# Kernel tuning notes

Measured on AMD Instinct MI355X. Metric: run time of the kernel, lower is better.

Reference implementation:

```python
import jax, jax.numpy as jnp
import numpy as np
from jax import lax

N = 19
ACT_DIM = 12
_SRC = np.array([0,1,2,3,4,5,6,7,8,9,10,11,12,13,14,15,16,17,18,1,2,3,4,5,6,7,8,9,10,11,12,13,14,15,16,17], dtype=np.int64)
_DST = np.array([1,2,3,4,5,6,7,8,9,10,11,12,13,14,15,16,17,18,17,0,1,2,3,4,5,6,7,8,9,10,11,12,13,14,15,16], dtype=np.int64)
SRC = jnp.asarray(_SRC)
DST = jnp.asarray(_DST)
# GAT/GCN in PyG add self-loops by default
SRC_SL = jnp.concatenate([SRC, jnp.arange(N)])
DST_SL = jnp.concatenate([DST, jnp.arange(N)])


def _lin(v, W, b=None):
    y = v @ W.T
    return y + b if b is not None else y


def _minmax(v):
    return (v - v.min()) / (v.max() - v.min())


def _conv(x, w, b, pad):
    y = lax.conv_general_dilated(x, w, (2, 2), [(pad, pad), (pad, pad)], dimension_numbers=('NCHW', 'OIHW', 'NCHW'))
    return y + b[None, :, None, None]


def _sage_layer(h, lw, lb, rw):
    # SAGEConv(aggr='add'): lin_l(sum_{j->i} x_j) + lin_r(x_i); lin_r has no bias
    agg = jax.ops.segment_sum(h[SRC], DST, num_segments=N)
    return agg @ lw.T + lb + h @ rw.T


def _gat(h, W, a_s, a_d, b):
    # GATConv heads=1, leaky_relu slope 0.2, softmax over incoming edges (incl. self-loop)
    hh = h @ W.T
    es, ed = hh @ a_s, hh @ a_d
    e = jax.nn.leaky_relu(es[SRC_SL] + ed[DST_SL], 0.2)
    m = jax.ops.segment_max(e, DST_SL, num_segments=N)
    ex = jnp.exp(e - m[DST_SL])
    den = jax.ops.segment_sum(ex, DST_SL, num_segments=N)
    alpha = ex / den[DST_SL]
    return jax.ops.segment_sum(alpha[:, None] * hh[SRC_SL], DST_SL, num_segments=N) + b


def _gcn(h, W, b):
    # GCNConv(improved=True): A_hat = A + 2I, D^{-1/2} A_hat D^{-1/2}
    hh = h @ W.T
    w_e = jnp.concatenate([jnp.ones(SRC.shape[0], jnp.float32), 2.0 * jnp.ones(N, jnp.float32)])
    deg = jax.ops.segment_sum(w_e, DST_SL, num_segments=N)
    dinv = lax.rsqrt(deg)
    norm = dinv[SRC_SL] * dinv[DST_SL] * w_e
    return jax.ops.segment_sum(norm[:, None] * hh[SRC_SL], DST_SL, num_segments=N) + b


def setup_inputs() -> dict:
    ks = iter(jax.random.split(jax.random.key(0), 64))
    def nrm(*shape):
        return jax.random.normal(next(ks), shape, jnp.float32) * 0.02
    d = dict(
        x=jax.random.normal(next(ks), (1, 128, 128), jnp.float32),
        state=jax.random.normal(next(ks), (20,), jnp.float32),
        x_graph=jax.random.normal(next(ks), (19,), jnp.float32),
        c1w=nrm(32, 1, 5, 5), c1b=nrm(32),
        c2w=nrm(32, 32, 5, 5), c2b=nrm(32),
        c3w=nrm(32, 32, 5, 5), c3b=nrm(32),
        fc0w=nrm(6000, 6272), fc0b=nrm(6000),
        fc1w=nrm(100, 6000), fc1b=nrm(100),
        fc2w=nrm(100, 20), fc2b=nrm(100),
        fc3w=nrm(100, 100), fc3b=nrm(100),
        sg1a_lw=nrm(1000, 1), sg1a_lb=nrm(1000), sg1a_rw=nrm(1000, 1),
        sg1b_lw=nrm(1000, 1000), sg1b_lb=nrm(1000), sg1b_rw=nrm(1000, 1000),
        gat2_w=nrm(1000, 1000), gat2_as=nrm(1000), gat2_ad=nrm(1000), gat2_b=nrm(1000),
        sg3a_lw=nrm(1000, 1000), sg3a_lb=nrm(1000), sg3a_rw=nrm(1000, 1000),
        sg3b_lw=nrm(1000, 1000), sg3b_lb=nrm(1000), sg3b_rw=nrm(1000, 1000),
        gat4_w=nrm(1000, 1000), gat4_as=nrm(1000), gat4_ad=nrm(1000), gat4_b=nrm(1000),
        gcn_w=nrm(1000, 1000), gcn_b=nrm(1000),
        fcg_w=nrm(100, 1000), fcg_b=nrm(100),
        fc4w=nrm(200, 300), fc4b=nrm(200),
        mu_w=nrm(ACT_DIM, 200), mu_b=nrm(ACT_DIM),
        log_sigma=jnp.zeros((ACT_DIM,), jnp.float32),
        cr_w=nrm(1, 200), cr_b=nrm(1),
    )
    return d


def reference(x, state, x_graph, c1w, c1b, c2w, c2b, c3w, c3b, fc0w, fc0b, fc1w, fc1b, fc2w, fc2b, fc3w, fc3b, sg1a_lw, sg1a_lb, sg1a_rw, sg1b_lw, sg1b_lb, sg1b_rw, gat2_w, gat2_as, gat2_ad, gat2_b, sg3a_lw, sg3a_lb, sg3a_rw, sg3b_lw, sg3b_lb, sg3b_rw, gat4_w, gat4_as, gat4_ad, gat4_b, gcn_w, gcn_b, fcg_w, fcg_b, fc4w, fc4b, mu_w, mu_b, log_sigma, cr_w, cr_b):
    relu = jax.nn.relu
    xc = x[None]                       # [1,1,128,128]
    xc = relu(_conv(xc, c1w, c1b, 1))  # [1,32,63,63]
    xc = relu(_conv(xc, c2w, c2b, 0))  # [1,32,30,30]
    xc = _conv(xc, c3w, c3b, 1)        # [1,32,14,14] (no relu after conv3 in source)
    v = xc.reshape(-1)                 # 6272
    v = _lin(_lin(v, fc0w, fc0b), fc1w, fc1b)
    n1 = _minmax(v)
    s = _lin(_lin(state, fc2w, fc2b), fc3w, fc3b)
    n2 = _minmax(s)
    h = x_graph[:, None]               # [19,1]
    h = relu(_sage_layer(h, sg1a_lw, sg1a_lb, sg1a_rw))   # GraphSAGE layer 1 (inner ReLU)
    h = relu(_sage_layer(h, sg1b_lw, sg1b_lb, sg1b_rw))   # layer 2, then outer ReLU (idempotent)
    h = relu(_gat(h, gat2_w, gat2_as, gat2_ad, gat2_b))
    h = relu(_sage_layer(h, sg3a_lw, sg3a_lb, sg3a_rw))
    h = relu(_sage_layer(h, sg3b_lw, sg3b_lb, sg3b_rw))
    h = relu(_gat(h, gat4_w, gat4_as, gat4_ad, gat4_b))
    h = _gcn(h, gcn_w, gcn_b)
    g = _lin(h.mean(0), fcg_w, fcg_b)
    n3 = _minmax(g)
    feats = _lin(jnp.concatenate([n1, n2, n3]), fc4w, fc4b)
    mu = jnp.tanh(_lin(feats, mu_w, mu_b))
    sigma = jnp.exp(log_sigma)
    value = _lin(feats, cr_w, cr_b)
    return (mu, sigma, value)
```

## Files before the change

kernel.cpp:

```cpp
#include <hip/hip_runtime.h>
#include <math.h>

#define DEV __device__ __forceinline__

constexpr int ESRC[36] = {0,1,2,3,4,5,6,7,8,9,10,11,12,13,14,15,16,17,18,1,2,3,4,5,6,7,8,9,10,11,12,13,14,15,16,17};
constexpr int EDST[36] = {1,2,3,4,5,6,7,8,9,10,11,12,13,14,15,16,17,18,17,0,1,2,3,4,5,6,7,8,9,10,11,12,13,14,15,16};
constexpr int SSRC[55] = {0,1,2,3,4,5,6,7,8,9,10,11,12,13,14,15,16,17,18,1,2,3,4,5,6,7,8,9,10,11,12,13,14,15,16,17,
                          0,1,2,3,4,5,6,7,8,9,10,11,12,13,14,15,16,17,18};
constexpr int SDST[55] = {1,2,3,4,5,6,7,8,9,10,11,12,13,14,15,16,17,18,17,0,1,2,3,4,5,6,7,8,9,10,11,12,13,14,15,16,
                          0,1,2,3,4,5,6,7,8,9,10,11,12,13,14,15,16,17,18};
constexpr float DINV[19] = {0.5773502691896258f,0.5f,0.5f,0.5f,0.5f,0.5f,0.5f,0.5f,0.5f,0.5f,
                            0.5f,0.5f,0.5f,0.5f,0.5f,0.5f,0.5f,0.5f,0.5773502691896258f};

constexpr int WS_PH  = 0;
constexpr int WS_C1  = 0;
constexpr int WS_C2  = 127008;
constexpr int WS_V   = 155808;
constexpr int WS_FC0 = 162080;
constexpr int WS_N1  = 168080;
constexpr int WS_N2  = 168180;
constexpr int WS_HA  = 168280;
constexpr int WS_HB  = 187280;
constexpr int WS_AGA = 206280;
constexpr int WS_FC0B= 206280;
constexpr int WS_GV  = 263280;
constexpr int WS_AL  = 264280;
constexpr int WS_N3  = 264280;
constexpr int WS_PB  = 264384;
constexpr int WS_PC  = 340384;
constexpr int WS_FC0C= 416384;
constexpr int WS_FC0D= 422384;

DEV float wredsum(float v){
  #pragma unroll
  for (int o = 32; o; o >>= 1) v += __shfl_xor(v, o);
  return v;
}
DEV float d4(float4 a, float4 b){ return a.x*b.x + a.y*b.y + a.z*b.z + a.w*b.w; }

template<int MODE>
DEV void sage_split(int blk, int tid, float* sm,
                    const float* __restrict__ hin, const float* __restrict__ pin,
                    const float* __restrict__ pbias, const float* __restrict__ agin,
                    const float* __restrict__ lw, const float* __restrict__ rw,
                    float* __restrict__ pout)
{
  const int cg = blk >> 2, kq = blk & 3;
  const int kb = kq*256;
  const int cntf = (kq < 3) ? 256 : 232;
  const int cnt4 = cntf >> 2;
  float* hS = sm;
  float* aS = sm + 19*256;
  if (MODE == 2){
    for (int c = tid; c < 19*256; c += 256){
      const int n = c >> 8, j = c & 255;
      if (j < cntf){
        const int i = kb + j;
        const float v = pin[n*1000+i] + pin[(19+n)*1000+i] + pin[(38+n)*1000+i]
                      + pin[(57+n)*1000+i] + pbias[i];
        hS[c] = fmaxf(v, 0.f);
      }
    }
  } else {
    for (int c = tid; c < 19*64; c += 256){
      const int n = c >> 6, j = c & 63;
      if (j < cnt4)
        ((float4*)hS)[n*64 + j] = *(const float4*)(hin + n*1000 + kb + 4*j);
    }
  }
  if (MODE == 0){
    for (int c = tid; c < 19*64; c += 256){
      const int n = c >> 6, j = c & 63;
      if (j < cnt4)
        ((float4*)aS)[n*64 + j] = *(const float4*)(agin + n*1000 + kb + 4*j);
    }
  }
  __syncthreads();
  if (MODE != 0){
    if (tid < cntf){
      float hv[19];
      #pragma unroll
      for (int n=0;n<19;++n) hv[n] = hS[n*256 + tid];
      float ag[19];
      #pragma unroll
      for (int n=0;n<19;++n) ag[n] = 0.f;
      #pragma unroll
      for (int e=0;e<36;++e) ag[EDST[e]] += hv[ESRC[e]];
      #pragma unroll
      for (int n=0;n<19;++n) aS[n*256 + tid] = ag[n];
    }
    __syncthreads();
  }
  const int lane = tid & 63, wv = tid >> 6;
  const int i0 = cg*8 + 2*wv, i1 = i0 + 1;
  float acc0[19], acc1[19];
  #pragma unroll
  for (int n=0;n<19;++n){ acc0[n]=0.f; acc1[n]=0.f; }
  if (lane < cnt4){
    const float4 wl0 = *((const float4*)(lw + i0*1000) + kq*64 + lane);
    const float4 wl1 = *((const float4*)(lw + i1*1000) + kq*64 + lane);
    const float4 wr0 = *((const float4*)(rw + i0*1000) + kq*64 + lane);
    const float4 wr1 = *((const float4*)(rw + i1*1000) + kq*64 + lane);
    const float4* h4 = (const float4*)hS;
    const float4* a4 = (const float4*)aS;
    #pragma unroll
    for (int n=0;n<19;++n){
      const float4 hv = h4[n*64+lane], av = a4[n*64+lane];
      acc0[n] = d4(wl0,av) + d4(wr0,hv);
      acc1[n] = d4(wl1,av) + d4(wr1,hv);
    }
  }
  #pragma unroll
  for (int n=0;n<19;++n){ acc0[n]=wredsum(acc0[n]); acc1[n]=wredsum(acc1[n]); }
  if (lane == 0){
    #pragma unroll
    for (int n=0;n<19;++n){
      pout[(kq*19+n)*1000 + i0] = acc0[n];
      pout[(kq*19+n)*1000 + i1] = acc1[n];
    }
  }
}

template<int MODE>
DEV void gatmat_split(int blk, int tid, float* sm,
                      const float* __restrict__ hin, const float* __restrict__ pin,
                      const float* __restrict__ pbias,
                      const float* __restrict__ W, float* __restrict__ pout)
{
  const int cg = blk >> 2, kq = blk & 3;
  const int kb = kq*256;
  const int cntf = (kq < 3) ? 256 : 232;
  const int cnt4 = cntf >> 2;
  float* hS = sm;
  if (MODE == 2){
    for (int c = tid; c < 19*256; c += 256){
      const int n = c >> 8, j = c & 255;
      if (j < cntf){
        const int i = kb + j;
        const float v = pin[n*1000+i] + pin[(19+n)*1000+i] + pin[(38+n)*1000+i]
                      + pin[(57+n)*1000+i] + pbias[i];
        hS[c] = fmaxf(v, 0.f);
      }
    }
  } else {
    for (int c = tid; c < 19*64; c += 256){
      const int n = c >> 6, j = c & 63;
      if (j < cnt4)
        ((float4*)hS)[n*64 + j] = *(const float4*)(hin + n*1000 + kb + 4*j);
    }
  }
  __syncthreads();
  const int lane = tid & 63, wv = tid >> 6;
  const int i0 = cg*8 + 2*wv, i1 = i0 + 1;
  float acc0[19], acc1[19];
  #pragma unroll
  for (int n=0;n<19;++n){ acc0[n]=0.f; acc1[n]=0.f; }
  if (lane < cnt4){
    const float4 w0 = *((const float4*)(W + i0*1000) + kq*64 + lane);
    const float4 w1 = *((const float4*)(W + i1*1000) + kq*64 + lane);
    const float4* h4 = (const float4*)hS;
    #pragma unroll
    for (int n=0;n<19;++n){
      const float4 hv = h4[n*64+lane];
      acc0[n] = d4(w0,hv);
      acc1[n] = d4(w1,hv);
    }
  }
  #pragma unroll
  for (int n=0;n<19;++n){ acc0[n]=wredsum(acc0[n]); acc1[n]=wredsum(acc1[n]); }
  if (lane == 0){
    #pragma unroll
    for (int n=0;n<19;++n){
      pout[(kq*19+n)*1000 + i0] = acc0[n];
      pout[(kq*19+n)*1000 + i1] = acc1[n];
    }
  }
}

__global__ __launch_bounds__(1024) void k_alpha(
    const float* __restrict__ ph, const float* __restrict__ as_,
    const float* __restrict__ ad_, float* __restrict__ alpha_out)
{
  __shared__ float red[608];
  __shared__ float s_es[19], s_ed[19], s_w[55], s_m[19], s_den[19];
  const int t = threadIdx.x, lane = t & 63, wv = t >> 6;
  const bool ok = t < 1000;
  const float asv = ok ? as_[t] : 0.f;
  const float adv = ok ? ad_[t] : 0.f;
  float es[19], ed[19];
  #pragma unroll
  for (int n=0;n<19;++n){
    float hh = 0.f;
    if (ok) hh = ph[n*1000+t] + ph[(19+n)*1000+t] + ph[(38+n)*1000+t] + ph[(57+n)*1000+t];
    es[n] = hh*asv; ed[n] = hh*adv;
  }
  #pragma unroll
  for (int n=0;n<19;++n){ es[n]=wredsum(es[n]); ed[n]=wredsum(ed[n]); }
  if (lane == 0){
    #pragma unroll
    for (int n=0;n<19;++n){ red[wv*38+n]=es[n]; red[wv*38+19+n]=ed[n]; }
  }
  __syncthreads();
  if (t < 38){
    float s = 0.f;
    #pragma unroll
    for (int w2=0; w2<16; ++w2) s += red[w2*38+t];
    if (t < 19) s_es[t] = s; else s_ed[t-19] = s;
  }
  __syncthreads();
  if (t < 55){
    float e = s_es[SSRC[t]] + s_ed[SDST[t]];
    s_w[t] = e > 0.f ? e : 0.2f*e;
  }
  __syncthreads();
  if (t < 19){
    float m = -1e30f;
    #pragma unroll
    for (int e=0;e<55;++e) if (SDST[e]==t) m = fmaxf(m, s_w[e]);
    float den = 0.f;
    #pragma unroll
    for (int e=0;e<55;++e) if (SDST[e]==t) den += expf(s_w[e]-m);
    s_m[t]=m; s_den[t]=den;
  }
  __syncthreads();
  if (t < 55) alpha_out[t] = expf(s_w[t]-s_m[SDST[t]]) / s_den[SDST[t]];
}

DEV void gagg(int blk, int tid, float* sm, const float* __restrict__ ph,
              const float* __restrict__ alpha, const float* __restrict__ bias,
              float* __restrict__ hout)
{
  if (tid < 55) sm[tid] = alpha[tid];
  __syncthreads();
  const int i = blk*256 + tid;
  if (i < 1000){
    float hv[19];
    #pragma unroll
    for (int n=0;n<19;++n)
      hv[n] = ph[n*1000+i] + ph[(19+n)*1000+i] + ph[(38+n)*1000+i] + ph[(57+n)*1000+i];
    float acc[19];
    #pragma unroll
    for (int n=0;n<19;++n) acc[n]=0.f;
    #pragma unroll
    for (int e=0;e<55;++e) acc[SDST[e]] += sm[e]*hv[SSRC[e]];
    const float bi = bias[i];
    #pragma unroll
    for (int n=0;n<19;++n) hout[n*1000+i] = fmaxf(acc[n]+bi, 0.f);
  }
}

__global__ __launch_bounds__(256) void k_ac_1(
    const float* __restrict__ x, const float* __restrict__ c1w, const float* __restrict__ c1b,
    const float* __restrict__ xg, const float* __restrict__ s1alw, const float* __restrict__ s1alb,
    const float* __restrict__ s1arw,
    const float* __restrict__ stt, const float* __restrict__ fc2w, const float* __restrict__ fc2b,
    const float* __restrict__ fc3w, const float* __restrict__ fc3b,
    float* __restrict__ ws)
{
  const int b = blockIdx.x, t = threadIdx.x;
  if (b < 497){
    const int idx = b*256 + t;
    if (idx < 127008){
      const int oc = idx/3969, r = idx - oc*3969, oy = r/63, ox = r - oy*63;
      const float* wp = c1w + oc*25;
      float acc = c1b[oc];
      #pragma unroll
      for (int ky=0;ky<5;++ky){
        const int iy = oy*2 - 1 + ky;
        if ((unsigned)iy < 128u){
          #pragma unroll
          for (int kx=0;kx<5;++kx){
            const int ix = ox*2 - 1 + kx;
            if ((unsigned)ix < 128u) acc += x[iy*128+ix]*wp[ky*5+kx];
          }
        }
      }
      ws[WS_C1+idx] = fmaxf(acc, 0.f);
    }
  } else if (b < 501){
    const int i = (b-497)*256 + t;
    if (i < 1000){
      float xv[19];
      #pragma unroll
      for (int n=0;n<19;++n) xv[n] = xg[n];
      float ag[19];
      #pragma unroll
      for (int n=0;n<19;++n) ag[n]=0.f;
      #pragma unroll
      for (int e=0;e<36;++e) ag[EDST[e]] += xv[ESRC[e]];
      const float lwv=s1alw[i], lbv=s1alb[i], rwv=s1arw[i];
      float hc[19];
      #pragma unroll
      for (int n=0;n<19;++n){
        hc[n] = fmaxf(lwv*ag[n] + lbv + rwv*xv[n], 0.f);
        ws[WS_HA+n*1000+i] = hc[n];
      }
      #pragma unroll
      for (int n=0;n<19;++n){
        float a=0.f;
        #pragma unroll
        for (int e=0;e<36;++e) if (EDST[e]==n) a += hc[ESRC[e]];
        ws[WS_AGA+n*1000+i] = a;
      }
    }
  } else {
    __shared__ float s1[100];
    if (t < 100){
      float acc = fc2b[t];
      #pragma unroll
      for (int k=0;k<20;++k) acc += fc2w[t*20+k]*stt[k];
      s1[t] = acc;
    }
    __syncthreads();
    if (t < 100){
      float acc = fc3b[t];
      for (int k=0;k<100;++k) acc += fc3w[t*100+k]*s1[k];
      ws[WS_N2+t] = acc;
    }
  }
}

__global__ __launch_bounds__(256) void k_ac_2(
    const float* __restrict__ c2w, const float* __restrict__ c2b,
    const float* __restrict__ s1blw, const float* __restrict__ s1blb, const float* __restrict__ s1brw,
    float* __restrict__ ws)
{
  __shared__ float sm[9728];
  const int b = blockIdx.x, t = threadIdx.x;
  if (b < 128){
    const int oc = b >> 2, q = b & 3;
    const int r0 = q*16;
    const int nout = (q < 3) ? 240 : 180;
    float* buf0 = sm; float* buf1 = sm + 4788;
    float rv[19];
    #pragma unroll
    for (int u=0; u<19; ++u){
      const int c = t + u*256; float v = 0.f;
      if (c < 4788){
        const int p = c/1197, r = c - p*1197, lr = r/63, xx = r - lr*63;
        const int iy = r0 + lr;
        if (iy < 63) v = ws[WS_C1 + p*3969 + iy*63 + xx];
      }
      rv[u] = v;
    }
    #pragma unroll
    for (int u=0; u<19; ++u){ const int c = t+u*256; if (c<4788) buf0[c]=rv[u]; }
    __syncthreads();
    const int oy_l = t/30, ox = t - oy_l*30;
    float acc = (t < nout) ? c2b[oc] : 0.f;
    for (int g=0; g<8; ++g){
      float* cur = (g&1) ? buf1 : buf0;
      if (g < 7){
        #pragma unroll
        for (int u=0; u<19; ++u){
          const int c = t + u*256; float v = 0.f;
          if (c < 4788){
            const int p = c/1197, r = c - p*1197, lr = r/63, xx = r - lr*63;
            const int iy = r0 + lr;
            if (iy < 63) v = ws[WS_C1 + (4*(g+1)+p)*3969 + iy*63 + xx];
          }
          rv[u] = v;
        }
      }
      if (t < nout){
        #pragma unroll
        for (int p=0;p<4;++p){
          const float* wp = c2w + (oc*32 + 4*g + p)*25;
          const float* ip = cur + p*1197 + (2*oy_l)*63 + 2*ox;
          #pragma unroll
          for (int ky=0;ky<5;++ky)
            #pragma unroll
            for (int kx=0;kx<5;++kx)
              acc += ip[ky*63+kx]*wp[ky*5+kx];
        }
      }
      if (g < 7){
        __syncthreads();
        float* nxt = (g&1) ? buf0 : buf1;
        #pragma unroll
        for (int u=0; u<19; ++u){ const int c = t+u*256; if (c<4788) nxt[c]=rv[u]; }
        __syncthreads();
      }
    }
    if (t < nout){
      const int oy = q*8 + oy_l;
      ws[WS_C2 + oc*900 + oy*30 + ox] = fmaxf(acc, 0.f);
    }
  } else {
    sage_split<0>(b-128, t, sm, ws+WS_HA, nullptr, nullptr, ws+WS_AGA, s1blw, s1brw, ws+WS_PB);
  }
}

__global__ __launch_bounds__(256) void k_ac_3(
    const float* __restrict__ c3w, const float* __restrict__ c3b,
    const float* __restrict__ s1blb, const float* __restrict__ g2w,
    float* __restrict__ ws)
{
  __shared__ float sm[7200];
  const int b = blockIdx.x, t = threadIdx.x;
  if (b < 32){
    const int oc = b;
    float* buf0 = sm; float* buf1 = sm + 3600;
    float rv[15];
    #pragma unroll
    for (int u=0; u<15; ++u){
      const int c = t + u*256;
      rv[u] = (c < 3600) ? ws[WS_C2 + c] : 0.f;
    }
    #pragma unroll
    for (int u=0; u<15; ++u){ const int c = t+u*256; if (c<3600) buf0[c]=rv[u]; }
    __syncthreads();
    const int oy = t/14, ox = t - oy*14;
    float acc = (t < 196) ? c3b[oc] : 0.f;
    for (int g=0; g<8; ++g){
      float* cur = (g&1) ? buf1 : buf0;
      if (g < 7){
        #pragma unroll
        for (int u=0; u<15; ++u){
          const int c = t + u*256;
          rv[u] = (c < 3600) ? ws[WS_C2 + (g+1)*3600 + c] : 0.f;
        }
      }
      if (t < 196){
        #pragma unroll
        for (int p=0;p<4;++p){
          const float* wp = c3w + (oc*32 + 4*g + p)*25;
          const float* ip = cur + p*900;
          #pragma unroll
          for (int ky=0;ky<5;++ky){
            const int iy = oy*2 - 1 + ky;
            if ((unsigned)iy < 30u){
              #pragma unroll
              for (int kx=0;kx<5;++kx){
                const int ix = ox*2 - 1 + kx;
                if ((unsigned)ix < 30u) acc += ip[iy*30+ix]*wp[ky*5+kx];
              }
            }
          }
        }
      }
      if (g < 7){
        __syncthreads();
        float* nxt = (g&1) ? buf0 : buf1;
        #pragma unroll
        for (int u=0; u<15; ++u){ const int c = t+u*256; if (c<3600) nxt[c]=rv[u]; }
        __syncthreads();
      }
    }
    if (t < 196) ws[WS_V + oc*196 + t] = acc;
  } else {
    gatmat_split<2>(b-32, t, sm, nullptr, ws+WS_PB, s1blb, g2w, ws+WS_PH);
  }
}

__global__ __launch_bounds__(256) void k_ac_4b(
    const float* __restrict__ g2b, float* __restrict__ ws)
{
  __shared__ float sm[64];
  gagg(blockIdx.x, threadIdx.x, sm, ws+WS_PH, ws+WS_AL, g2b, ws+WS_HA);
}

__global__ __launch_bounds__(256) void k_ac_4(
    const float* __restrict__ fc0w, float* __restrict__ ws)
{
  const int b = blockIdx.x, t = threadIdx.x;
  const int lane = t & 63, wv = t >> 6;
  const int rq = b >> 2, q = b & 3;
  const int row = rq*4 + wv;
  const float4* vr = (const float4*)(ws + WS_V) + q*392;
  const float4* wr = (const float4*)(fc0w) + (size_t)row*1568 + q*392;
  float4 wreg[6];
  #pragma unroll
  for (int u=0; u<6; ++u) wreg[u] = wr[u*64 + lane];
  float4 wtail;
  if (lane < 8) wtail = wr[384 + lane];
  float acc = 0.f;
  #pragma unroll
  for (int u=0; u<6; ++u) acc += d4(wreg[u], vr[u*64 + lane]);
  if (lane < 8) acc += d4(wtail, vr[384 + lane]);
  acc = wredsum(acc);
  if (lane == 0){
    float* pout = ws + (q==0 ? WS_FC0 : q==1 ? WS_FC0B : q==2 ? WS_FC0C : WS_FC0D);
    pout[row] = acc;
  }
}

__global__ __launch_bounds__(256) void k_ac_5(
    const float* __restrict__ fc1w, const float* __restrict__ fc1b,
    const float* __restrict__ fc0b,
    const float* __restrict__ s3alw, const float* __restrict__ s3arw,
    float* __restrict__ ws)
{
  __shared__ float sm[9728];
  const int b = blockIdx.x, t = threadIdx.x;
  if (b < 100){
    const int row = b, lane = t & 63, wv = t >> 6;
    const float4* wr = (const float4*)(fc1w + row*6000);
    const float4* p0 = (const float4*)(ws + WS_FC0);
    const float4* p1 = (const float4*)(ws + WS_FC0B);
    const float4* p2 = (const float4*)(ws + WS_FC0C);
    const float4* p3 = (const float4*)(ws + WS_FC0D);
    const float4* bb = (const float4*)fc0b;
    float acc = 0.f;
    #pragma unroll
    for (int u=0; u<6; ++u){
      const int j = t + u*256;
      if (j < 1500){
        const float4 a0=p0[j], a1=p1[j], a2=p2[j], a3=p3[j], bv=bb[j];
        const float4 s = make_float4(a0.x+a1.x+a2.x+a3.x+bv.x,
                                     a0.y+a1.y+a2.y+a3.y+bv.y,
                                     a0.z+a1.z+a2.z+a3.z+bv.z,
                                     a0.w+a1.w+a2.w+a3.w+bv.w);
        acc += d4(wr[j], s);
      }
    }
    acc = wredsum(acc);
    if (lane == 0) sm[wv] = acc;
    __syncthreads();
    if (t == 0) ws[WS_N1+row] = sm[0]+sm[1]+sm[2]+sm[3] + fc1b[row];
  } else {
    sage_split<1>(b-100, t, sm, ws+WS_HA, nullptr, nullptr, nullptr, s3alw, s3arw, ws+WS_PB);
  }
}

__global__ __launch_bounds__(256) void k_ac_6(
    const float* __restrict__ s3alb, const float* __restrict__ s3blw, const float* __restrict__ s3brw,
    float* __restrict__ ws)
{
  __shared__ float sm[9728];
  sage_split<2>(blockIdx.x, threadIdx.x, sm, nullptr, ws+WS_PB, s3alb, nullptr, s3blw, s3brw, ws+WS_PC);
}

__global__ __launch_bounds__(256) void k_ac_7(
    const float* __restrict__ s3blb, const float* __restrict__ g4w, float* __restrict__ ws)
{
  __shared__ float sm[4864];
  gatmat_split<2>(blockIdx.x, threadIdx.x, sm, nullptr, ws+WS_PC, s3blb, g4w, ws+WS_PH);
}

__global__ __launch_bounds__(256) void k_ac_8(
    const float* __restrict__ g4b, float* __restrict__ ws)
{
  __shared__ float sm[64];
  gagg(blockIdx.x, threadIdx.x, sm, ws+WS_PH, ws+WS_AL, g4b, ws+WS_HB);
}

__global__ __launch_bounds__(256) void k_ac_9(
    const float* __restrict__ gw, float* __restrict__ ws)
{
  __shared__ float sm[4864];
  gatmat_split<3>(blockIdx.x, threadIdx.x, sm, ws+WS_HB, nullptr, nullptr, gw, ws+WS_PB);
}

__global__ __launch_bounds__(256) void k_ac_10(
    const float* __restrict__ gb, float* __restrict__ ws)
{
  const int i = blockIdx.x*256 + threadIdx.x;
  if (i < 1000){
    float c[19];
    #pragma unroll
    for (int m=0;m<19;++m) c[m] = 2.f*DINV[m]*DINV[m];
    #pragma unroll
    for (int e=0;e<36;++e) c[ESRC[e]] += DINV[ESRC[e]]*DINV[EDST[e]];
    float s = gb[i];
    #pragma unroll
    for (int m=0;m<19;++m){
      const float hh = ws[WS_PB + m*1000 + i] + ws[WS_PB + (19+m)*1000 + i]
                     + ws[WS_PB + (38+m)*1000 + i] + ws[WS_PB + (57+m)*1000 + i];
      s += (c[m]*(1.f/19.f))*hh;
    }
    ws[WS_GV+i] = s;
  }
}

__global__ __launch_bounds__(256) void k_ac_11(
    const float* __restrict__ fcgw, const float* __restrict__ fcgb, float* __restrict__ ws)
{
  __shared__ float sm[4];
  const int b = blockIdx.x, t = threadIdx.x, lane = t & 63, wv = t >> 6;
  const float4* wr = (const float4*)(fcgw + b*1000);
  const float4* vr = (const float4*)(ws + WS_GV);
  float acc = (t < 250) ? d4(wr[t], vr[t]) : 0.f;
  acc = wredsum(acc);
  if (lane == 0) sm[wv] = acc;
  __syncthreads();
  if (t == 0) ws[WS_N3+b] = sm[0]+sm[1]+sm[2]+sm[3] + fcgb[b];
}

__global__ __launch_bounds__(512) void k_ac_head(
    const float* __restrict__ fc4w, const float* __restrict__ fc4b,
    const float* __restrict__ muw, const float* __restrict__ mub,
    const float* __restrict__ ls,  const float* __restrict__ crw, const float* __restrict__ crb,
    float* __restrict__ ws, float* __restrict__ out)
{
  __shared__ float f[300];
  __shared__ float mnmx[6];
  __shared__ float feats[200];
  const int t = threadIdx.x, lane = t & 63, wv = t >> 6;
  if (t < 100)       f[t] = ws[WS_N1 + t];
  else if (t < 200)  f[t] = ws[WS_N2 + t - 100];
  else if (t < 300)  f[t] = ws[WS_N3 + t - 200];
  if (t >= 300 && t < 312) out[t - 288] = expf(ls[t-300]);
  __syncthreads();
  if (wv < 3){
    const int base = wv*100;
    const float v  = f[base + lane];
    const float v2 = (lane < 36) ? f[base + 64 + lane] : v;
    float mn = fminf(v, v2), mx = fmaxf(v, v2);
    #pragma unroll
    for (int o=32;o;o>>=1){ mn = fminf(mn, __shfl_xor(mn,o)); mx = fmaxf(mx, __shfl_xor(mx,o)); }
    if (lane == 0){ mnmx[wv*2]=mn; mnmx[wv*2+1]=mx; }
  }
  __syncthreads();
  if (t < 300){
    const int c = t/100;
    f[t] = (f[t]-mnmx[c*2])/(mnmx[c*2+1]-mnmx[c*2]);
  }
  __syncthreads();
  for (int rr=0; rr<25; ++rr){
    const int row = wv*25 + rr;
    const float* wp = fc4w + row*300;
    float acc = 0.f;
    #pragma unroll
    for (int it=0; it<5; ++it){
      const int k = it*64 + lane;
      if (k < 300) acc += wp[k]*f[k];
    }
    acc = wredsum(acc);
    if (lane == 0) feats[row] = acc + fc4b[row];
  }
  __syncthreads();
  #pragma unroll
  for (int rr=0; rr<2; ++rr){
    const int row = wv + rr*8;
    if (row < 12){
      const float* wp = muw + row*200;
      float a = 0.f;
      #pragma unroll
      for (int it=0; it<4; ++it){
        const int k = it*64 + lane;
        if (k < 200) a += wp[k]*feats[k];
      }
      a = wredsum(a);
      if (lane == 0) out[row] = tanhf(a + mub[row]);
    } else if (rr == 1 && wv == 4){
      float a = 0.f;
      #pragma unroll
      for (int it=0; it<4; ++it){
        const int k = it*64 + lane;
        if (k < 200) a += crw[k]*feats[k];
      }
      a = wredsum(a);
      if (lane == 0) out[24] = a + crb[0];
    }
  }
}

extern "C" void kernel_launch(void* const* d_in, const int* in_sizes, int n_in,
                              void* d_out, int out_size, void* d_ws, size_t ws_size,
                              hipStream_t stream)
{
  (void)in_sizes; (void)n_in; (void)out_size; (void)ws_size;
  const float* x     = (const float*)d_in[0];
  const float* stt   = (const float*)d_in[1];
  const float* xg    = (const float*)d_in[2];
  const float* c1w   = (const float*)d_in[3];
  const float* c1b   = (const float*)d_in[4];
  const float* c2w   = (const float*)d_in[5];
  const float* c2b   = (const float*)d_in[6];
  const float* c3w   = (const float*)d_in[7];
  const float* c3b   = (const float*)d_in[8];
  const float* fc0w  = (const float*)d_in[9];
  const float* fc0b  = (const float*)d_in[10];
  const float* fc1w  = (const float*)d_in[11];
  const float* fc1b  = (const float*)d_in[12];
  const float* fc2w  = (const float*)d_in[13];
  const float* fc2b  = (const float*)d_in[14];
  const float* fc3w  = (const float*)d_in[15];
  const float* fc3b  = (const float*)d_in[16];
  const float* s1alw = (const float*)d_in[17];
  const float* s1alb = (const float*)d_in[18];
  const float* s1arw = (const float*)d_in[19];
  const float* s1blw = (const float*)d_in[20];
  const float* s1blb = (const float*)d_in[21];
  const float* s1brw = (const float*)d_in[22];
  const float* g2w   = (const float*)d_in[23];
  const float* g2as  = (const float*)d_in[24];
  const float* g2ad  = (const float*)d_in[25];
  const float* g2b   = (const float*)d_in[26];
  const float* s3alw = (const float*)d_in[27];
  const float* s3alb = (const float*)d_in[28];
  const float* s3arw = (const float*)d_in[29];
  const float* s3blw = (const float*)d_in[30];
  const float* s3blb = (const float*)d_in[31];
  const float* s3brw = (const float*)d_in[32];
  const float* g4w   = (const float*)d_in[33];
  const float* g4as  = (const float*)d_in[34];
  const float* g4ad  = (const float*)d_in[35];
  const float* g4b   = (const float*)d_in[36];
  const float* gcnw  = (const float*)d_in[37];
  const float* gcnb  = (const float*)d_in[38];
  const float* fcgw  = (const float*)d_in[39];
  const float* fcgb  = (const float*)d_in[40];
  const float* fc4w  = (const float*)d_in[41];
  const float* fc4b  = (const float*)d_in[42];
  const float* muw   = (const float*)d_in[43];
  const float* mub   = (const float*)d_in[44];
  const float* lsig  = (const float*)d_in[45];
  const float* crw   = (const float*)d_in[46];
  const float* crb   = (const float*)d_in[47];
  float* ws  = (float*)d_ws;
  float* out = (float*)d_out;

  k_ac_1 <<<dim3(502), dim3(256), 0, stream>>>(x, c1w, c1b, xg, s1alw, s1alb, s1arw,
                                               stt, fc2w, fc2b, fc3w, fc3b, ws);
  k_ac_2 <<<dim3(628), dim3(256), 0, stream>>>(c2w, c2b, s1blw, s1blb, s1brw, ws);
  k_ac_3 <<<dim3(532), dim3(256), 0, stream>>>(c3w, c3b, s1blb, g2w, ws);
  k_alpha<<<dim3(1), dim3(1024), 0, stream>>>(ws+WS_PH, g2as, g2ad, ws+WS_AL);
  k_ac_4b<<<dim3(4), dim3(256), 0, stream>>>(g2b, ws);
  k_ac_4 <<<dim3(6000), dim3(256), 0, stream>>>(fc0w, ws);
  k_ac_5 <<<dim3(600), dim3(256), 0, stream>>>(fc1w, fc1b, fc0b, s3alw, s3arw, ws);
  k_ac_6 <<<dim3(500), dim3(256), 0, stream>>>(s3alb, s3blw, s3brw, ws);
  k_ac_7 <<<dim3(500), dim3(256), 0, stream>>>(s3blb, g4w, ws);
  k_alpha<<<dim3(1), dim3(1024), 0, stream>>>(ws+WS_PH, g4as, g4ad, ws+WS_AL);
  k_ac_8 <<<dim3(4),   dim3(256), 0, stream>>>(g4b, ws);
  k_ac_9 <<<dim3(500), dim3(256), 0, stream>>>(gcnw, ws);
  k_ac_10<<<dim3(4),   dim3(256), 0, stream>>>(gcnb, ws);
  k_ac_11<<<dim3(100), dim3(256), 0, stream>>>(fcgw, fcgb, ws);
  k_ac_head<<<dim3(1), dim3(512), 0, stream>>>(fc4w, fc4b, muw, mub, lsig, crw, crb, ws, out);
}
```

Before: 274.2 us.

## Fuse GNN stages across fewer kernel launches and recompute GAT alpha per block

The schedule drops from fifteen launches to eight. The separate alpha kernels are folded into the consuming blocks, with each block recomputing the attention coefficients in shared memory. SAGE layer 1 is fused into the layer-2 matmul and the GCN/fcg stages are merged into the head kernel. The aim is to cut launch overhead and the serialization between tiny single-block kernels. In exchange there is redundant alpha computation in every block, and the head's 1000x100 GEMV now runs on a single block.

```diff
diff --git a/kernel.cpp b/kernel.cpp
--- a/kernel.cpp
+++ b/kernel.cpp
@@ -12,7 +12,6 @@
 constexpr float DINV[19] = {0.5773502691896258f,0.5f,0.5f,0.5f,0.5f,0.5f,0.5f,0.5f,0.5f,0.5f,
                             0.5f,0.5f,0.5f,0.5f,0.5f,0.5f,0.5f,0.5f,0.5773502691896258f};
 
-constexpr int WS_PH  = 0;
 constexpr int WS_C1  = 0;
 constexpr int WS_C2  = 127008;
 constexpr int WS_V   = 155808;
@@ -20,16 +19,12 @@
 constexpr int WS_N1  = 168080;
 constexpr int WS_N2  = 168180;
 constexpr int WS_HA  = 168280;
-constexpr int WS_HB  = 187280;
-constexpr int WS_AGA = 206280;
 constexpr int WS_FC0B= 206280;
-constexpr int WS_GV  = 263280;
-constexpr int WS_AL  = 264280;
-constexpr int WS_N3  = 264280;
 constexpr int WS_PB  = 264384;
 constexpr int WS_PC  = 340384;
 constexpr int WS_FC0C= 416384;
 constexpr int WS_FC0D= 422384;
+constexpr int WS_PH2 = 428384;
 
 DEV float wredsum(float v){
   #pragma unroll
@@ -40,12 +35,11 @@
 
 template<int MODE>
 DEV void sage_split(int blk, int tid, float* sm,
-                    const float* __restrict__ hin, const float* __restrict__ pin,
-                    const float* __restrict__ pbias, const float* __restrict__ agin,
-                    const float* __restrict__ lw, const float* __restrict__ rw,
-                    float* __restrict__ pout)
-{
-  const int cg = blk >> 2, kq = blk & 3;
+                    const float* hin, const float* pin,
+                    const float* pbias,
+                    const float* lw, const float* rw, float* pout)
+{
+  const int cg_ = blk >> 2, kq = blk & 3;
   const int kb = kq*256;
   const int cntf = (kq < 3) ? 256 : 232;
   const int cnt4 = cntf >> 2;
@@ -68,31 +62,22 @@
         ((float4*)hS)[n*64 + j] = *(const float4*)(hin + n*1000 + kb + 4*j);
     }
   }
-  if (MODE == 0){
-    for (int c = tid; c < 19*64; c += 256){
-      const int n = c >> 6, j = c & 63;
-      if (j < cnt4)
-        ((float4*)aS)[n*64 + j] = *(const float4*)(agin + n*1000 + kb + 4*j);
-    }
-  }
-  __syncthreads();
-  if (MODE != 0){
-    if (tid < cntf){
-      float hv[19];
-      #pragma unroll
-      for (int n=0;n<19;++n) hv[n] = hS[n*256 + tid];
-      float ag[19];
-      #pragma unroll
-      for (int n=0;n<19;++n) ag[n] = 0.f;
-      #pragma unroll
-      for (int e=0;e<36;++e) ag[EDST[e]] += hv[ESRC[e]];
-      #pragma unroll
-      for (int n=0;n<19;++n) aS[n*256 + tid] = ag[n];
-    }
-    __syncthreads();
-  }
+  __syncthreads();
+  if (tid < cntf){
+    float hv[19];
+    #pragma unroll
+    for (int n=0;n<19;++n) hv[n] = hS[n*256 + tid];
+    float ag[19];
+    #pragma unroll
+    for (int n=0;n<19;++n) ag[n] = 0.f;
+    #pragma unroll
+    for (int e=0;e<36;++e) ag[EDST[e]] += hv[ESRC[e]];
+    #pragma unroll
+    for (int n=0;n<19;++n) aS[n*256 + tid] = ag[n];
+  }
+  __syncthreads();
   const int lane = tid & 63, wv = tid >> 6;
-  const int i0 = cg*8 + 2*wv, i1 = i0 + 1;
+  const int i0 = cg_*8 + 2*wv, i1 = i0 + 1;
   float acc0[19], acc1[19];
   #pragma unroll
   for (int n=0;n<19;++n){ acc0[n]=0.f; acc1[n]=0.f; }
@@ -121,13 +106,75 @@
   }
 }
 
+DEV void sage1b_fused(int blk, int tid, float* sm, const float* xg,
+                      const float* alw, const float* alb, const float* arw,
+                      const float* lw, const float* rw, float* pout)
+{
+  const int cg_ = blk >> 2, kq = blk & 3;
+  const int kb = kq*256;
+  const int cntf = (kq < 3) ? 256 : 232;
+  const int cnt4 = cntf >> 2;
+  float* hS = sm;
+  float* aS = sm + 19*256;
+  float xv[19];
+  #pragma unroll
+  for (int n=0;n<19;++n) xv[n] = xg[n];
+  float ag0[19];
+  #pragma unroll
+  for (int n=0;n<19;++n) ag0[n] = 0.f;
+  #pragma unroll
+  for (int e=0;e<36;++e) ag0[EDST[e]] += xv[ESRC[e]];
+  if (tid < cntf){
+    const int i = kb + tid;
+    const float a = alw[i], bb = alb[i], r = arw[i];
+    float hv[19];
+    #pragma unroll
+    for (int n=0;n<19;++n){ hv[n] = fmaxf(a*ag0[n] + bb + r*xv[n], 0.f); hS[n*256+tid] = hv[n]; }
+    float ag[19];
+    #pragma unroll
+    for (int n=0;n<19;++n) ag[n] = 0.f;
+    #pragma unroll
+    for (int e=0;e<36;++e) ag[EDST[e]] += hv[ESRC[e]];
+    #pragma unroll
+    for (int n=0;n<19;++n) aS[n*256+tid] = ag[n];
+  }
+  __syncthreads();
+  const int lane = tid & 63, wv = tid >> 6;
+  const int i0 = cg_*8 + 2*wv, i1 = i0 + 1;
+  float acc0[19], acc1[19];
+  #pragma unroll
+  for (int n=0;n<19;++n){ acc0[n]=0.f; acc1[n]=0.f; }
+  if (lane < cnt4){
+    const float4 wl0 = *((const float4*)(lw + i0*1000) + kq*64 + lane);
+    const float4 wl1 = *((const float4*)(lw + i1*1000) + kq*64 + lane);
+    const float4 wr0 = *((const float4*)(rw + i0*1000) + kq*64 + lane);
+    const float4 wr1 = *((const float4*)(rw + i1*1000) + kq*64 + lane);
+    const float4* h4 = (const float4*)hS;
+    const float4* a4 = (const float4*)aS;
+    #pragma unroll
+    for (int n=0;n<19;++n){
+      const float4 hv = h4[n*64+lane], av = a4[n*64+lane];
+      acc0[n] = d4(wl0,av) + d4(wr0,hv);
+      acc1[n] = d4(wl1,av) + d4(wr1,hv);
+    }
+  }
+  #pragma unroll
+  for (int n=0;n<19;++n){ acc0[n]=wredsum(acc0[n]); acc1[n]=wredsum(acc1[n]); }
+  if (lane == 0){
+    #pragma unroll
+    for (int n=0;n<19;++n){
+      pout[(kq*19+n)*1000 + i0] = acc0[n];
+      pout[(kq*19+n)*1000 + i1] = acc1[n];
+    }
+  }
+}
+
 template<int MODE>
 DEV void gatmat_split(int blk, int tid, float* sm,
-                      const float* __restrict__ hin, const float* __restrict__ pin,
-                      const float* __restrict__ pbias,
-                      const float* __restrict__ W, float* __restrict__ pout)
-{
-  const int cg = blk >> 2, kq = blk & 3;
+                      const float* hin, const float* pin, const float* pbias,
+                      const float* W, float* pout)
+{
+  const int cg_ = blk >> 2, kq = blk & 3;
   const int kb = kq*256;
   const int cntf = (kq < 3) ? 256 : 232;
   const int cnt4 = cntf >> 2;
@@ -151,7 +198,7 @@
   }
   __syncthreads();
   const int lane = tid & 63, wv = tid >> 6;
-  const int i0 = cg*8 + 2*wv, i1 = i0 + 1;
+  const int i0 = cg_*8 + 2*wv, i1 = i0 + 1;
   float acc0[19], acc1[19];
   #pragma unroll
   for (int n=0;n<19;++n){ acc0[n]=0.f; acc1[n]=0.f; }
@@ -177,62 +224,55 @@
   }
 }
 
-__global__ __launch_bounds__(1024) void k_alpha(
-    const float* __restrict__ ph, const float* __restrict__ as_,
-    const float* __restrict__ ad_, float* __restrict__ alpha_out)
-{
-  __shared__ float red[608];
-  __shared__ float s_es[19], s_ed[19], s_w[55], s_m[19], s_den[19];
-  const int t = threadIdx.x, lane = t & 63, wv = t >> 6;
-  const bool ok = t < 1000;
-  const float asv = ok ? as_[t] : 0.f;
-  const float adv = ok ? ad_[t] : 0.f;
+DEV void alpha_sm(int t, float* sm, const float* ph, const float* as_,
+                  const float* ad_)
+{
+  const int lane = t & 63, wv = t >> 6;
   float es[19], ed[19];
   #pragma unroll
-  for (int n=0;n<19;++n){
-    float hh = 0.f;
-    if (ok) hh = ph[n*1000+t] + ph[(19+n)*1000+t] + ph[(38+n)*1000+t] + ph[(57+n)*1000+t];
-    es[n] = hh*asv; ed[n] = hh*adv;
+  for (int n=0;n<19;++n){ es[n]=0.f; ed[n]=0.f; }
+  for (int k = t; k < 1000; k += 256){
+    const float asv = as_[k], adv = ad_[k];
+    #pragma unroll
+    for (int n=0;n<19;++n){
+      const float hh = ph[n*1000+k] + ph[(19+n)*1000+k] + ph[(38+n)*1000+k] + ph[(57+n)*1000+k];
+      es[n] += hh*asv; ed[n] += hh*adv;
+    }
   }
   #pragma unroll
   for (int n=0;n<19;++n){ es[n]=wredsum(es[n]); ed[n]=wredsum(ed[n]); }
   if (lane == 0){
     #pragma unroll
-    for (int n=0;n<19;++n){ red[wv*38+n]=es[n]; red[wv*38+19+n]=ed[n]; }
-  }
-  __syncthreads();
-  if (t < 38){
-    float s = 0.f;
-    #pragma unroll
-    for (int w2=0; w2<16; ++w2) s += red[w2*38+t];
-    if (t < 19) s_es[t] = s; else s_ed[t-19] = s;
-  }
+    for (int n=0;n<19;++n){ sm[wv*38+n]=es[n]; sm[wv*38+19+n]=ed[n]; }
+  }
+  __syncthreads();
+  if (t < 38) sm[152+t] = sm[t] + sm[38+t] + sm[76+t] + sm[114+t];
   __syncthreads();
   if (t < 55){
-    float e = s_es[SSRC[t]] + s_ed[SDST[t]];
-    s_w[t] = e > 0.f ? e : 0.2f*e;
+    float e = sm[152+SSRC[t]] + sm[171+SDST[t]];
+    sm[200+t] = e > 0.f ? e : 0.2f*e;
   }
   __syncthreads();
   if (t < 19){
     float m = -1e30f;
     #pragma unroll
-    for (int e=0;e<55;++e) if (SDST[e]==t) m = fmaxf(m, s_w[e]);
+    for (int e=0;e<55;++e) if (SDST[e]==t) m = fmaxf(m, sm[200+e]);
     float den = 0.f;
     #pragma unroll
-    for (int e=0;e<55;++e) if (SDST[e]==t) den += expf(s_w[e]-m);
-    s_m[t]=m; s_den[t]=den;
-  }
-  __syncthreads();
-  if (t < 55) alpha_out[t] = expf(s_w[t]-s_m[SDST[t]]) / s_den[SDST[t]];
-}
-
-DEV void gagg(int blk, int tid, float* sm, const float* __restrict__ ph,
-              const float* __restrict__ alpha, const float* __restrict__ bias,
-              float* __restrict__ hout)
-{
-  if (tid < 55) sm[tid] = alpha[tid];
-  __syncthreads();
-  const int i = blk*256 + tid;
+    for (int e=0;e<55;++e) if (SDST[e]==t) den += expf(sm[200+e]-m);
+    sm[260+t]=m; sm[280+t]=den;
+  }
+  __syncthreads();
+  if (t < 55) sm[320+t] = expf(sm[200+t]-sm[260+SDST[t]]) / sm[280+SDST[t]];
+  __syncthreads();
+}
+
+DEV void gat_fin_task(int blk, int t, float* sm, const float* ph,
+                      const float* as_, const float* ad_,
+                      const float* bias, float* hout)
+{
+  alpha_sm(t, sm, ph, as_, ad_);
+  const int i = blk*256 + t;
   if (i < 1000){
     float hv[19];
     #pragma unroll
@@ -242,230 +282,209 @@
     #pragma unroll
     for (int n=0;n<19;++n) acc[n]=0.f;
     #pragma unroll
-    for (int e=0;e<55;++e) acc[SDST[e]] += sm[e]*hv[SSRC[e]];
+    for (int e=0;e<55;++e) acc[SDST[e]] += sm[320+e]*hv[SSRC[e]];
     const float bi = bias[i];
     #pragma unroll
     for (int n=0;n<19;++n) hout[n*1000+i] = fmaxf(acc[n]+bi, 0.f);
   }
 }
 
-__global__ __launch_bounds__(256) void k_ac_1(
-    const float* __restrict__ x, const float* __restrict__ c1w, const float* __restrict__ c1b,
-    const float* __restrict__ xg, const float* __restrict__ s1alw, const float* __restrict__ s1alb,
-    const float* __restrict__ s1arw,
-    const float* __restrict__ stt, const float* __restrict__ fc2w, const float* __restrict__ fc2b,
-    const float* __restrict__ fc3w, const float* __restrict__ fc3b,
-    float* __restrict__ ws)
-{
-  const int b = blockIdx.x, t = threadIdx.x;
-  if (b < 497){
-    const int idx = b*256 + t;
-    if (idx < 127008){
-      const int oc = idx/3969, r = idx - oc*3969, oy = r/63, ox = r - oy*63;
-      const float* wp = c1w + oc*25;
-      float acc = c1b[oc];
-      #pragma unroll
-      for (int ky=0;ky<5;++ky){
-        const int iy = oy*2 - 1 + ky;
-        if ((unsigned)iy < 128u){
-          #pragma unroll
-          for (int kx=0;kx<5;++kx){
-            const int ix = ox*2 - 1 + kx;
-            if ((unsigned)ix < 128u) acc += x[iy*128+ix]*wp[ky*5+kx];
-          }
+DEV void gcn_fused_task(int blk, int t, float* sm, const float* ph,
+                        const float* as_, const float* ad_, const float* bias,
+                        const float* W, float* pout)
+{
+  alpha_sm(t, sm, ph, as_, ad_);
+  const int cg_ = blk >> 2, kq = blk & 3;
+  const int kb = kq*256;
+  const int cntf = (kq < 3) ? 256 : 232;
+  const int cnt4 = cntf >> 2;
+  float* hS = sm + 384;
+  if (t < cntf){
+    const int i = kb + t;
+    float hv[19];
+    #pragma unroll
+    for (int n=0;n<19;++n)
+      hv[n] = ph[n*1000+i] + ph[(19+n)*1000+i] + ph[(38+n)*1000+i] + ph[(57+n)*1000+i];
+    float acc[19];
+    #pragma unroll
+    for (int n=0;n<19;++n) acc[n]=0.f;
+    #pragma unroll
+    for (int e=0;e<55;++e) acc[SDST[e]] += sm[320+e]*hv[SSRC[e]];
+    const float bi = bias[i];
+    #pragma unroll
+    for (int n=0;n<19;++n) hS[n*256+t] = fmaxf(acc[n]+bi, 0.f);
+  }
+  __syncthreads();
+  const int lane = t & 63, wv = t >> 6;
+  const int i0 = cg_*8 + 2*wv, i1 = i0 + 1;
+  float acc0[19], acc1[19];
+  #pragma unroll
+  for (int n=0;n<19;++n){ acc0[n]=0.f; acc1[n]=0.f; }
+  if (lane < cnt4){
+    const float4 w0 = *((const float4*)(W + i0*1000) + kq*64 + lane);
+    const float4 w1 = *((const float4*)(W + i1*1000) + kq*64 + lane);
+    const float4* h4 = (const float4*)hS;
+    #pragma unroll
+    for (int n=0;n<19;++n){
+      const float4 hv = h4[n*64+lane];
+      acc0[n] = d4(w0,hv);
+      acc1[n] = d4(w1,hv);
+    }
+  }
+  #pragma unroll
+  for (int n=0;n<19;++n){ acc0[n]=wredsum(acc0[n]); acc1[n]=wredsum(acc1[n]); }
+  if (lane == 0){
+    #pragma unroll
+    for (int n=0;n<19;++n){
+      pout[(kq*19+n)*1000 + i0] = acc0[n];
+      pout[(kq*19+n)*1000 + i1] = acc1[n];
+    }
+  }
+}
+
+DEV void conv1_task(int task, int t, const float* x, const float* c1w,
+                    const float* c1b, float* ws)
+{
+  const int idx = task*256 + t;
+  if (idx < 127008){
+    const int oc = idx/3969, r = idx - oc*3969, oy = r/63, ox = r - oy*63;
+    const float* wp = c1w + oc*25;
+    float acc = c1b[oc];
+    #pragma unroll
+    for (int ky=0;ky<5;++ky){
+      const int iy = oy*2 - 1 + ky;
+      if ((unsigned)iy < 128u){
+        #pragma unroll
+        for (int kx=0;kx<5;++kx){
+          const int ix = ox*2 - 1 + kx;
+          if ((unsigned)ix < 128u) acc += x[iy*128+ix]*wp[ky*5+kx];
         }
       }
-      ws[WS_C1+idx] = fmaxf(acc, 0.f);
-    }
-  } else if (b < 501){
-    const int i = (b-497)*256 + t;
-    if (i < 1000){
-      float xv[19];
+    }
+    ws[WS_C1+idx] = fmaxf(acc, 0.f);
+  }
+}
+
+DEV void conv2_task(int task, int t, float* sm, const float* c2w,
+                    const float* c2b, float* ws)
+{
+  const int oc = task >> 2, q = task & 3;
+  const int r0 = q*16;
+  const int nout = (q < 3) ? 240 : 180;
+  float* buf0 = sm; float* buf1 = sm + 4788;
+  float rv[19];
+  #pragma unroll
+  for (int u=0; u<19; ++u){
+    const int c = t + u*256; float v = 0.f;
+    if (c < 4788){
+      const int p = c/1197, r = c - p*1197, lr = r/63, xx = r - lr*63;
+      const int iy = r0 + lr;
+      if (iy < 63) v = ws[WS_C1 + p*3969 + iy*63 + xx];
+    }
+    rv[u] = v;
+  }
+  #pragma unroll
+  for (int u=0; u<19; ++u){ const int c = t+u*256; if (c<4788) buf0[c]=rv[u]; }
+  __syncthreads();
+  const int oy_l = t/30, ox = t - oy_l*30;
+  float acc = (t < nout) ? c2b[oc] : 0.f;
+  for (int g=0; g<8; ++g){
+    float* cur = (g&1) ? buf1 : buf0;
+    if (g < 7){
       #pragma unroll
-      for (int n=0;n<19;++n) xv[n] = xg[n];
-      float ag[19];
+      for (int u=0; u<19; ++u){
+        const int c = t + u*256; float v = 0.f;
+        if (c < 4788){
+          const int p = c/1197, r = c - p*1197, lr = r/63, xx = r - lr*63;
+          const int iy = r0 + lr;
+          if (iy < 63) v = ws[WS_C1 + (4*(g+1)+p)*3969 + iy*63 + xx];
+        }
+        rv[u] = v;
+      }
+    }
+    if (t < nout){
       #pragma unroll
-      for (int n=0;n<19;++n) ag[n]=0.f;
+      for (int p=0;p<4;++p){
+        const float* wp = c2w + (oc*32 + 4*g + p)*25;
+        const float* ip = cur + p*1197 + (2*oy_l)*63 + 2*ox;
+        #pragma unroll
+        for (int ky=0;ky<5;++ky)
+          #pragma unroll
+          for (int kx=0;kx<5;++kx)
+            acc += ip[ky*63+kx]*wp[ky*5+kx];
+      }
+    }
+    if (g < 7){
+      __syncthreads();
+      float* nxt = (g&1) ? buf0 : buf1;
       #pragma unroll
-      for (int e=0;e<36;++e) ag[EDST[e]] += xv[ESRC[e]];
-      const float lwv=s1alw[i], lbv=s1alb[i], rwv=s1arw[i];
-      float hc[19];
+      for (int u=0; u<19; ++u){ const int c = t+u*256; if (c<4788) nxt[c]=rv[u]; }
+      __syncthreads();
+    }
+  }
+  if (t < nout){
+    const int oy = q*8 + oy_l;
+    ws[WS_C2 + oc*900 + oy*30 + ox] = fmaxf(acc, 0.f);
+  }
+}
+
+DEV void conv3_task(int oc, int t, float* sm, const float* c3w,
+                    const float* c3b, float* ws)
+{
+  float* buf0 = sm; float* buf1 = sm + 3600;
+  float rv[15];
+  #pragma unroll
+  for (int u=0; u<15; ++u){
+    const int c = t + u*256;
+    rv[u] = (c < 3600) ? ws[WS_C2 + c] : 0.f;
+  }
+  #pragma unroll
+  for (int u=0; u<15; ++u){ const int c = t+u*256; if (c<3600) buf0[c]=rv[u]; }
+  __syncthreads();
+  const int oy = t/14, ox = t - oy*14;
+  float acc = (t < 196) ? c3b[oc] : 0.f;
+  for (int g=0; g<8; ++g){
+    float* cur = (g&1) ? buf1 : buf0;
+    if (g < 7){
       #pragma unroll
-      for (int n=0;n<19;++n){
-        hc[n] = fmaxf(lwv*ag[n] + lbv + rwv*xv[n], 0.f);
-        ws[WS_HA+n*1000+i] = hc[n];
+      for (int u=0; u<15; ++u){
+        const int c = t + u*256;
+        rv[u] = (c < 3600) ? ws[WS_C2 + (g+1)*3600 + c] : 0.f;
       }
+    }
+    if (t < 196){
       #pragma unroll
-      for (int n=0;n<19;++n){
-        float a=0.f;
+      for (int p=0;p<4;++p){
+        const float* wp = c3w + (oc*32 + 4*g + p)*25;
+        const float* ip = cur + p*900;
         #pragma unroll
-        for (int e=0;e<36;++e) if (EDST[e]==n) a += hc[ESRC[e]];
-        ws[WS_AGA+n*1000+i] = a;
-      }
-    }
-  } else {
-    __shared__ float s1[100];
-    if (t < 100){
-      float acc = fc2b[t];
-      #pragma unroll
-      for (int k=0;k<20;++k) acc += fc2w[t*20+k]*stt[k];
-      s1[t] = acc;
-    }
-    __syncthreads();
-    if (t < 100){
-      float acc = fc3b[t];
-      for (int k=0;k<100;++k) acc += fc3w[t*100+k]*s1[k];
-      ws[WS_N2+t] = acc;
-    }
-  }
-}
-
-__global__ __launch_bounds__(256) void k_ac_2(
-    const float* __restrict__ c2w, const float* __restrict__ c2b,
-    const float* __restrict__ s1blw, const float* __restrict__ s1blb, const float* __restrict__ s1brw,
-    float* __restrict__ ws)
-{
-  __shared__ float sm[9728];
-  const int b = blockIdx.x, t = threadIdx.x;
-  if (b < 128){
-    const int oc = b >> 2, q = b & 3;
-    const int r0 = q*16;
-    const int nout = (q < 3) ? 240 : 180;
-    float* buf0 = sm; float* buf1 = sm + 4788;
-    float rv[19];
-    #pragma unroll
-    for (int u=0; u<19; ++u){
-      const int c = t + u*256; float v = 0.f;
-      if (c < 4788){
-        const int p = c/1197, r = c - p*1197, lr = r/63, xx = r - lr*63;
-        const int iy = r0 + lr;
-        if (iy < 63) v = ws[WS_C1 + p*3969 + iy*63 + xx];
-      }
-      rv[u] = v;
-    }
-    #pragma unroll
-    for (int u=0; u<19; ++u){ const int c = t+u*256; if (c<4788) buf0[c]=rv[u]; }
-    __syncthreads();
-    const int oy_l = t/30, ox = t - oy_l*30;
-    float acc = (t < nout) ? c2b[oc] : 0.f;
-    for (int g=0; g<8; ++g){
-      float* cur = (g&1) ? buf1 : buf0;
-      if (g < 7){
-        #pragma unroll
-        for (int u=0; u<19; ++u){
-          const int c = t + u*256; float v = 0.f;
-          if (c < 4788){
-            const int p = c/1197, r = c - p*1197, lr = r/63, xx = r - lr*63;
-            const int iy = r0 + lr;
-            if (iy < 63) v = ws[WS_C1 + (4*(g+1)+p)*3969 + iy*63 + xx];
-          }
-          rv[u] = v;
-        }
-      }
-      if (t < nout){
-        #pragma unroll
-        for (int p=0;p<4;++p){
-          const float* wp = c2w + (oc*32 + 4*g + p)*25;
-          const float* ip = cur + p*1197 + (2*oy_l)*63 + 2*ox;
-          #pragma unroll
-          for (int ky=0;ky<5;++ky)
+        for (int ky=0;ky<5;++ky){
+          const int iy = oy*2 - 1 + ky;
+          if ((unsigned)iy < 30u){
             #pragma unroll
-            for (int kx=0;kx<5;++kx)
-              acc += ip[ky*63+kx]*wp[ky*5+kx];
-        }
-      }
-      if (g < 7){
-        __syncthreads();
-        float* nxt = (g&1) ? buf0 : buf1;
-        #pragma unroll
-        for (int u=0; u<19; ++u){ const int c = t+u*256; if (c<4788) nxt[c]=rv[u]; }
-        __syncthreads();
-      }
-    }
-    if (t < nout){
-      const int oy = q*8 + oy_l;
-      ws[WS_C2 + oc*900 + oy*30 + ox] = fmaxf(acc, 0.f);
-    }
-  } else {
-    sage_split<0>(b-128, t, sm, ws+WS_HA, nullptr, nullptr, ws+WS_AGA, s1blw, s1brw, ws+WS_PB);
-  }
-}
-
-__global__ __launch_bounds__(256) void k_ac_3(
-    const float* __restrict__ c3w, const float* __restrict__ c3b,
-    const float* __restrict__ s1blb, const float* __restrict__ g2w,
-    float* __restrict__ ws)
-{
-  __shared__ float sm[7200];
-  const int b = blockIdx.x, t = threadIdx.x;
-  if (b < 32){
-    const int oc = b;
-    float* buf0 = sm; float* buf1 = sm + 3600;
-    float rv[15];
-    #pragma unroll
-    for (int u=0; u<15; ++u){
-      const int c = t + u*256;
-      rv[u] = (c < 3600) ? ws[WS_C2 + c] : 0.f;
-    }
-    #pragma unroll
-    for (int u=0; u<15; ++u){ const int c = t+u*256; if (c<3600) buf0[c]=rv[u]; }
-    __syncthreads();
-    const int oy = t/14, ox = t - oy*14;
-    float acc = (t < 196) ? c3b[oc] : 0.f;
-    for (int g=0; g<8; ++g){
-      float* cur = (g&1) ? buf1 : buf0;
-      if (g < 7){
-        #pragma unroll
-        for (int u=0; u<15; ++u){
-          const int c = t + u*256;
-          rv[u] = (c < 3600) ? ws[WS_C2 + (g+1)*3600 + c] : 0.f;
-        }
-      }
-      if (t < 196){
-        #pragma unroll
-        for (int p=0;p<4;++p){
-          const float* wp = c3w + (oc*32 + 4*g + p)*25;
-          const float* ip = cur + p*900;
-          #pragma unroll
-          for (int ky=0;ky<5;++ky){
-            const int iy = oy*2 - 1 + ky;
-            if ((unsigned)iy < 30u){
-              #pragma unroll
-              for (int kx=0;kx<5;++kx){
-                const int ix = ox*2 - 1 + kx;
-                if ((unsigned)ix < 30u) acc += ip[iy*30+ix]*wp[ky*5+kx];
-              }
+            for (int kx=0;kx<5;++kx){
+              const int ix = ox*2 - 1 + kx;
+              if ((unsigned)ix < 30u) acc += ip[iy*30+ix]*wp[ky*5+kx];
             }
           }
         }
       }
-      if (g < 7){
-        __syncthreads();
-        float* nxt = (g&1) ? buf0 : buf1;
-        #pragma unroll
-        for (int u=0; u<15; ++u){ const int c = t+u*256; if (c<3600) nxt[c]=rv[u]; }
-        __syncthreads();
-      }
-    }
-    if (t < 196) ws[WS_V + oc*196 + t] = acc;
-  } else {
-    gatmat_split<2>(b-32, t, sm, nullptr, ws+WS_PB, s1blb, g2w, ws+WS_PH);
-  }
-}
-
-__global__ __launch_bounds__(256) void k_ac_4b(
-    const float* __restrict__ g2b, float* __restrict__ ws)
-{
-  __shared__ float sm[64];
-  gagg(blockIdx.x, threadIdx.x, sm, ws+WS_PH, ws+WS_AL, g2b, ws+WS_HA);
-}
-
-__global__ __launch_bounds__(256) void k_ac_4(
-    const float* __restrict__ fc0w, float* __restrict__ ws)
-{
-  const int b = blockIdx.x, t = threadIdx.x;
+    }
+    if (g < 7){
+      __syncthreads();
+      float* nxt = (g&1) ? buf0 : buf1;
+      #pragma unroll
+      for (int u=0; u<15; ++u){ const int c = t+u*256; if (c<3600) nxt[c]=rv[u]; }
+      __syncthreads();
+    }
+  }
+  if (t < 196) ws[WS_V + oc*196 + t] = acc;
+}
+
+DEV void fc0_task(int task, int t, const float* fc0w, float* ws)
+{
   const int lane = t & 63, wv = t >> 6;
-  const int rq = b >> 2, q = b & 3;
+  const int rq = task >> 2, q = task & 3;
   const int row = rq*4 + wv;
   const float4* vr = (const float4*)(ws + WS_V) + q*392;
   const float4* wr = (const float4*)(fc0w) + (size_t)row*1568 + q*392;
@@ -485,13 +504,77 @@
   }
 }
 
+__global__ __launch_bounds__(256) void k_ac_1(
+    const float* __restrict__ x, const float* __restrict__ c1w, const float* __restrict__ c1b,
+    const float* __restrict__ xg,
+    const float* __restrict__ s1alw, const float* __restrict__ s1alb, const float* __restrict__ s1arw,
+    const float* __restrict__ s1blw, const float* __restrict__ s1brw,
+    const float* __restrict__ stt, const float* __restrict__ fc2w, const float* __restrict__ fc2b,
+    const float* __restrict__ fc3w, const float* __restrict__ fc3b,
+    float* __restrict__ ws)
+{
+  __shared__ __align__(16) float sm[9728];
+  const int b = blockIdx.x, t = threadIdx.x;
+  if (b < 497){
+    conv1_task(b, t, x, c1w, c1b, ws);
+  } else if (b < 997){
+    sage1b_fused(b-497, t, sm, xg, s1alw, s1alb, s1arw, s1blw, s1brw, ws+WS_PB);
+  } else {
+    if (t < 100){
+      float acc = fc2b[t];
+      #pragma unroll
+      for (int k=0;k<20;++k) acc += fc2w[t*20+k]*stt[k];
+      sm[t] = acc;
+    }
+    __syncthreads();
+    if (t < 100){
+      float acc = fc3b[t];
+      for (int k=0;k<100;++k) acc += fc3w[t*100+k]*sm[k];
+      ws[WS_N2+t] = acc;
+    }
+  }
+}
+
+__global__ __launch_bounds__(256) void k_ac_2(
+    const float* __restrict__ c2w, const float* __restrict__ c2b,
+    const float* __restrict__ s1blb, const float* __restrict__ g2w,
+    float* __restrict__ ws)
+{
+  __shared__ __align__(16) float sm[9728];
+  const int b = blockIdx.x, t = threadIdx.x;
+  if (b < 128) conv2_task(b, t, sm, c2w, c2b, ws);
+  else gatmat_split<2>(b-128, t, sm, nullptr, ws+WS_PB, s1blb, g2w, ws+WS_PH2);
+}
+
+__global__ __launch_bounds__(256) void k_ac_3(
+    const float* __restrict__ c3w, const float* __restrict__ c3b,
+    const float* __restrict__ g2as, const float* __restrict__ g2ad, const float* __restrict__ g2b,
+    float* __restrict__ ws)
+{
+  __shared__ __align__(16) float sm[7200];
+  const int b = blockIdx.x, t = threadIdx.x;
+  if (b < 32) conv3_task(b, t, sm, c3w, c3b, ws);
+  else gat_fin_task(b-32, t, sm, ws+WS_PH2, g2as, g2ad, g2b, ws+WS_HA);
+}
+
+__global__ __launch_bounds__(256) void k_ac_4(
+    const float* __restrict__ fc0w,
+    const float* __restrict__ s3alw, const float* __restrict__ s3arw,
+    float* __restrict__ ws)
+{
+  __shared__ __align__(16) float sm[9728];
+  const int b = blockIdx.x, t = threadIdx.x;
+  if (b < 6000) fc0_task(b, t, fc0w, ws);
+  else sage_split<1>(b-6000, t, sm, ws+WS_HA, nullptr, nullptr, s3alw, s3arw, ws+WS_PB);
+}
+
 __global__ __launch_bounds__(256) void k_ac_5(
     const float* __restrict__ fc1w, const float* __restrict__ fc1b,
     const float* __restrict__ fc0b,
-    const float* __restrict__ s3alw, const float* __restrict__ s3arw,
+    const float* __restrict__ s3alb, const float* __restrict__ s3blw, const float* __restrict__ s3brw,
     float* __restrict__ ws)
 {
-  __shared__ float sm[9728];
+  __shared__ __align__(16) float sm[9728];
   const int b = blockIdx.x, t = threadIdx.x;
   if (b < 100){
     const int row = b, lane = t & 63, wv = t >> 6;
@@ -507,10 +590,8 @@
       const int j = t + u*256;
       if (j < 1500){
         const float4 a0=p0[j], a1=p1[j], a2=p2[j], a3=p3[j], bv=bb[j];
-        const float4 s = make_float4(a0.x+a1.x+a2.x+a3.x+bv.x,
-                                     a0.y+a1.y+a2.y+a3.y+bv.y,
-                                     a0.z+a1.z+a2.z+a3.z+bv.z,
-                                     a0.w+a1.w+a2.w+a3.w+bv.w);
+        const float4 s = make_float4(a0.x+a1.x+a2.x+a3.x+bv.x, a0.y+a1.y+a2.y+a3.y+bv.y,
+                                     a0.z+a1.z+a2.z+a3.z+bv.z, a0.w+a1.w+a2.w+a3.w+bv.w);
         acc += d4(wr[j], s);
       }
     }
@@ -519,137 +600,99 @@
     __syncthreads();
     if (t == 0) ws[WS_N1+row] = sm[0]+sm[1]+sm[2]+sm[3] + fc1b[row];
   } else {
-    sage_split<1>(b-100, t, sm, ws+WS_HA, nullptr, nullptr, nullptr, s3alw, s3arw, ws+WS_PB);
+    sage_split<2>(b-100, t, sm, nullptr, ws+WS_PB, s3alb, s3blw, s3brw, ws+WS_PC);
   }
 }
 
 __global__ __launch_bounds__(256) void k_ac_6(
-    const float* __restrict__ s3alb, const float* __restrict__ s3blw, const float* __restrict__ s3brw,
-    float* __restrict__ ws)
-{
-  __shared__ float sm[9728];
-  sage_split<2>(blockIdx.x, threadIdx.x, sm, nullptr, ws+WS_PB, s3alb, nullptr, s3blw, s3brw, ws+WS_PC);
+    const float* __restrict__ s3blb, const float* __restrict__ g4w, float* __restrict__ ws)
+{
+  __shared__ __align__(16) float sm[4864];
+  gatmat_split<2>(blockIdx.x, threadIdx.x, sm, nullptr, ws+WS_PC, s3blb, g4w, ws+WS_PH2);
 }
 
 __global__ __launch_bounds__(256) void k_ac_7(
-    const float* __restrict__ s3blb, const float* __restrict__ g4w, float* __restrict__ ws)
-{
-  __shared__ float sm[4864];
-  gatmat_split<2>(blockIdx.x, threadIdx.x, sm, nullptr, ws+WS_PC, s3blb, g4w, ws+WS_PH);
-}
-
-__global__ __launch_bounds__(256) void k_ac_8(
-    const float* __restrict__ g4b, float* __restrict__ ws)
-{
-  __shared__ float sm[64];
-  gagg(blockIdx.x, threadIdx.x, sm, ws+WS_PH, ws+WS_AL, g4b, ws+WS_HB);
-}
-
-__global__ __launch_bounds__(256) void k_ac_9(
-    const float* __restrict__ gw, float* __restrict__ ws)
-{
-  __shared__ float sm[4864];
-  gatmat_split<3>(blockIdx.x, threadIdx.x, sm, ws+WS_HB, nullptr, nullptr, gw, ws+WS_PB);
-}
-
-__global__ __launch_bounds__(256) void k_ac_10(
-    const float* __restrict__ gb, float* __restrict__ ws)
-{
-  const int i = blockIdx.x*256 + threadIdx.x;
-  if (i < 1000){
-    float c[19];
-    #pragma unroll
-    for (int m=0;m<19;++m) c[m] = 2.f*DINV[m]*DINV[m];
-    #pragma unroll
-    for (int e=0;e<36;++e) c[ESRC[e]] += DINV[ESRC[e]]*DINV[EDST[e]];
-    float s = gb[i];
+    const float* __restrict__ g4as, const float* __restrict__ g4ad, const float* __restrict__ g4b,
+    const float* __restrict__ gcnw, float* __restrict__ ws)
+{
+  __shared__ __align__(16) float sm[5248];
+  gcn_fused_task(blockIdx.x, threadIdx.x, sm, ws+WS_PH2, g4as, g4ad, g4b, gcnw, ws+WS_PB);
+}
+
+__global__ __launch_bounds__(256) void k_ac_head(
+    const float* __restrict__ gcnb, const float* __restrict__ fcgw, const float* __restrict__ fcgb,
+    const float* __restrict__ fc4w, const float* __restrict__ fc4b,
+    const float* __restrict__ muw, const float* __restrict__ mub,
+    const float* __restrict__ lsig, const float* __restrict__ crw, const float* __restrict__ crb,
+    float* __restrict__ ws, float* __restrict__ out)
+{
+  __shared__ __align__(16) float sm[1808];
+  const int t = threadIdx.x, lane = t & 63, wv = t >> 6;
+  __shared__ __align__(16) float gv[1000];
+  float cc[19];
+  #pragma unroll
+  for (int m=0;m<19;++m) cc[m] = 2.f*DINV[m]*DINV[m];
+  #pragma unroll
+  for (int e=0;e<36;++e) cc[ESRC[e]] += DINV[ESRC[e]]*DINV[EDST[e]];
+  for (int i = t; i < 1000; i += 256){
+    float s = gcnb[i];
     #pragma unroll
     for (int m=0;m<19;++m){
       const float hh = ws[WS_PB + m*1000 + i] + ws[WS_PB + (19+m)*1000 + i]
                      + ws[WS_PB + (38+m)*1000 + i] + ws[WS_PB + (57+m)*1000 + i];
-      s += (c[m]*(1.f/19.f))*hh;
-    }
-    ws[WS_GV+i] = s;
-  }
-}
-
-__global__ __launch_bounds__(256) void k_ac_11(
-    const float* __restrict__ fcgw, const float* __restrict__ fcgb, float* __restrict__ ws)
-{
-  __shared__ float sm[4];
-  const int b = blockIdx.x, t = threadIdx.x, lane = t & 63, wv = t >> 6;
-  const float4* wr = (const float4*)(fcgw + b*1000);
-  const float4* vr = (const float4*)(ws + WS_GV);
-  float acc = (t < 250) ? d4(wr[t], vr[t]) : 0.f;
-  acc = wredsum(acc);
-  if (lane == 0) sm[wv] = acc;
-  __syncthreads();
-  if (t == 0) ws[WS_N3+b] = sm[0]+sm[1]+sm[2]+sm[3] + fcgb[b];
-}
-
-__global__ __launch_bounds__(512) void k_ac_head(
-    const float* __restrict__ fc4w, const float* __restrict__ fc4b,
-    const float* __restrict__ muw, const float* __restrict__ mub,
-    const float* __restrict__ ls,  const float* __restrict__ crw, const float* __restrict__ crb,
-    float* __restrict__ ws, float* __restrict__ out)
-{
-  __shared__ float f[300];
-  __shared__ float mnmx[6];
-  __shared__ float feats[200];
-  const int t = threadIdx.x, lane = t & 63, wv = t >> 6;
-  if (t < 100)       f[t] = ws[WS_N1 + t];
-  else if (t < 200)  f[t] = ws[WS_N2 + t - 100];
-  else if (t < 300)  f[t] = ws[WS_N3 + t - 200];
-  if (t >= 300 && t < 312) out[t - 288] = expf(ls[t-300]);
+      s += (cc[m]*(1.f/19.f))*hh;
+    }
+    gv[i] = s;
+  }
+  __syncthreads();
+  for (int r = wv; r < 100; r += 4){
+    const float4* wr4 = (const float4*)(fcgw + r*1000);
+    const float4* gv4 = (const float4*)gv;
+    float acc = 0.f;
+    for (int j = lane; j < 250; j += 64) acc += d4(wr4[j], gv4[j]);
+    acc = wredsum(acc);
+    if (lane == 0) sm[1024+r] = acc + fcgb[r];
+  }
+  __syncthreads();
+  for (int c = t; c < 300; c += 256){
+    float v = (c < 100) ? ws[WS_N1+c] : (c < 200) ? ws[WS_N2+c-100] : sm[1024+c-200];
+    sm[1200+c] = v;
+  }
   __syncthreads();
   if (wv < 3){
-    const int base = wv*100;
-    const float v  = f[base + lane];
-    const float v2 = (lane < 36) ? f[base + 64 + lane] : v;
+    const int base = 1200 + wv*100;
+    const float v  = sm[base + lane];
+    const float v2 = (lane < 36) ? sm[base + 64 + lane] : v;
     float mn = fminf(v, v2), mx = fmaxf(v, v2);
     #pragma unroll
     for (int o=32;o;o>>=1){ mn = fminf(mn, __shfl_xor(mn,o)); mx = fmaxf(mx, __shfl_xor(mx,o)); }
-    if (lane == 0){ mnmx[wv*2]=mn; mnmx[wv*2+1]=mx; }
-  }
-  __syncthreads();
-  if (t < 300){
-    const int c = t/100;
-    f[t] = (f[t]-mnmx[c*2])/(mnmx[c*2+1]-mnmx[c*2]);
-  }
-  __syncthreads();
-  for (int rr=0; rr<25; ++rr){
-    const int row = wv*25 + rr;
-    const float* wp = fc4w + row*300;
+    if (lane == 0){ sm[1500+wv*2]=mn; sm[1501+wv*2]=mx; }
+  }
+  __syncthreads();
+  for (int c = t; c < 300; c += 256){
+    const int g = c/100;
+    sm[1200+c] = (sm[1200+c]-sm[1500+g*2])/(sm[1501+g*2]-sm[1500+g*2]);
+  }
+  __syncthreads();
+  for (int r = wv; r < 200; r += 4){
+    const float* wp = fc4w + r*300;
     float acc = 0.f;
-    #pragma unroll
-    for (int it=0; it<5; ++it){
-      const int k = it*64 + lane;
-      if (k < 300) acc += wp[k]*f[k];
-    }
+    for (int k = lane; k < 300; k += 64) acc += wp[k]*sm[1200+k];
     acc = wredsum(acc);
-    if (lane == 0) feats[row] = acc + fc4b[row];
-  }
-  __syncthreads();
-  #pragma unroll
-  for (int rr=0; rr<2; ++rr){
-    const int row = wv + rr*8;
-    if (row < 12){
-      const float* wp = muw + row*200;
+    if (lane == 0) sm[1600+r] = acc + fc4b[r];
+  }
+  __syncthreads();
+  if (t >= 12 && t < 24) out[t] = expf(lsig[t-12]);
+  for (int r = wv; r < 16; r += 4){
+    if (r < 12){
+      const float* wp = muw + r*200;
       float a = 0.f;
-      #pragma unroll
-      for (int it=0; it<4; ++it){
-        const int k = it*64 + lane;
-        if (k < 200) a += wp[k]*feats[k];
-      }
+      for (int k = lane; k < 200; k += 64) a += wp[k]*sm[1600+k];
       a = wredsum(a);
-      if (lane == 0) out[row] = tanhf(a + mub[row]);
-    } else if (rr == 1 && wv == 4){
+      if (lane == 0) out[r] = tanhf(a + mub[r]);
+    } else if (r == 12){
       float a = 0.f;
-      #pragma unroll
-      for (int it=0; it<4; ++it){
-        const int k = it*64 + lane;
-        if (k < 200) a += crw[k]*feats[k];
-      }
+      for (int k = lane; k < 200; k += 64) a += crw[k]*sm[1600+k];
       a = wredsum(a);
       if (lane == 0) out[24] = a + crb[0];
     }
@@ -712,20 +755,14 @@
   float* ws  = (float*)d_ws;
   float* out = (float*)d_out;
 
-  k_ac_1 <<<dim3(502), dim3(256), 0, stream>>>(x, c1w, c1b, xg, s1alw, s1alb, s1arw,
-                                               stt, fc2w, fc2b, fc3w, fc3b, ws);
-  k_ac_2 <<<dim3(628), dim3(256), 0, stream>>>(c2w, c2b, s1blw, s1blb, s1brw, ws);
-  k_ac_3 <<<dim3(532), dim3(256), 0, stream>>>(c3w, c3b, s1blb, g2w, ws);
-  k_alpha<<<dim3(1), dim3(1024), 0, stream>>>(ws+WS_PH, g2as, g2ad, ws+WS_AL);
-  k_ac_4b<<<dim3(4), dim3(256), 0, stream>>>(g2b, ws);
-  k_ac_4 <<<dim3(6000), dim3(256), 0, stream>>>(fc0w, ws);
-  k_ac_5 <<<dim3(600), dim3(256), 0, stream>>>(fc1w, fc1b, fc0b, s3alw, s3arw, ws);
-  k_ac_6 <<<dim3(500), dim3(256), 0, stream>>>(s3alb, s3blw, s3brw, ws);
-  k_ac_7 <<<dim3(500), dim3(256), 0, stream>>>(s3blb, g4w, ws);
-  k_alpha<<<dim3(1), dim3(1024), 0, stream>>>(ws+WS_PH, g4as, g4ad, ws+WS_AL);
-  k_ac_8 <<<dim3(4),   dim3(256), 0, stream>>>(g4b, ws);
-  k_ac_9 <<<dim3(500), dim3(256), 0, stream>>>(gcnw, ws);
-  k_ac_10<<<dim3(4),   dim3(256), 0, stream>>>(gcnb, ws);
-  k_ac_11<<<dim3(100), dim3(256), 0, stream>>>(fcgw, fcgb, ws);
-  k_ac_head<<<dim3(1), dim3(512), 0, stream>>>(fc4w, fc4b, muw, mub, lsig, crw, crb, ws, out);
-}
+  k_ac_1 <<<dim3(998),  dim3(256), 0, stream>>>(x, c1w, c1b, xg, s1alw, s1alb, s1arw,
+                                                s1blw, s1brw, stt, fc2w, fc2b, fc3w, fc3b, ws);
+  k_ac_2 <<<dim3(628),  dim3(256), 0, stream>>>(c2w, c2b, s1blb, g2w, ws);
+  k_ac_3 <<<dim3(36),   dim3(256), 0, stream>>>(c3w, c3b, g2as, g2ad, g2b, ws);
+  k_ac_4 <<<dim3(6500), dim3(256), 0, stream>>>(fc0w, s3alw, s3arw, ws);
+  k_ac_5 <<<dim3(600),  dim3(256), 0, stream>>>(fc1w, fc1b, fc0b, s3alb, s3blw, s3brw, ws);
+  k_ac_6 <<<dim3(500),  dim3(256), 0, stream>>>(s3blb, g4w, ws);
+  k_ac_7 <<<dim3(500),  dim3(256), 0, stream>>>(g4as, g4ad, g4b, gcnw, ws);
+  k_ac_head<<<dim3(1),  dim3(256), 0, stream>>>(gcnb, fcgw, fcgb, fc4w, fc4b,
+                                                muw, mub, lsig, crw, crb, ws, out);
+}
```

Result: slower. 413.9 us (+51.0%).
